# Optimization experiments

Hardware: AMD Instinct MI355X
Metric: run time of the kernel (lower is better)

## Reference

```python
import jax, jax.numpy as jnp
import numpy as np

B = 16384
S0, S1 = 7, 7
NB, NC = 2, 20
WC, WN = 5.0, 0.5  # weight_coord, weight_noobject
D = NB * 5 + NC  # 30


def setup_inputs() -> dict:
    key = jax.random.key(0)
    k1, k2, k3, k4 = jax.random.split(key, 4)
    predication = jax.random.normal(k1, (B, S0 * S1 * D), dtype=jnp.float32)
    grid = jax.random.randint(k2, (B, S0, S1), 0, 2, dtype=jnp.int32)
    tbox = jax.random.uniform(k3, (B, S0, S1, 4), dtype=jnp.float32)
    # keep target w,h strictly positive (real boxes), offsets in [0,1)
    tbox = tbox.at[..., 2:].set(0.05 + 0.9 * tbox[..., 2:])
    tcls = jax.random.randint(k4, (B, S0, S1), 0, NC, dtype=jnp.int32)
    return {"predication": predication, "grid": grid, "tbox": tbox, "tcls": tcls}


def _yolo_loss(predication, grid, tbox, tcls):
    pred = predication.reshape(B, S0, S1, D)
    conf = jax.nn.sigmoid(pred[..., :NB])                                  # (B,S0,S1,NB)
    pb = jax.nn.sigmoid(pred[..., NB:5 * NB]).reshape(B, S0, S1, NB, 4)    # (B,S0,S1,NB,4)
    cls = jax.nn.softmax(pred[..., 5 * NB:], axis=-1)                      # (B,S0,S1,NC)

    # cell coordinates: x = column index, y = row index (matches the [1,0] swap in torch code)
    xg = jnp.arange(S1, dtype=pred.dtype)[None, None, :]   # (1,1,S1)
    yg = jnp.arange(S0, dtype=pred.dtype)[None, :, None]   # (1,S0,1)

    tox, toy, tw, th = tbox[..., 0], tbox[..., 1], tbox[..., 2], tbox[..., 3]
    tcx = (xg + tox) / S0
    tcy = (yg + toy) / S1

    pcx = (xg[..., None] + pb[..., 0]) / S0   # (B,S0,S1,NB)
    pcy = (yg[..., None] + pb[..., 1]) / S1
    pw, ph = pb[..., 2], pb[..., 3]

    # IOU of each predicted box vs the cell's target box (same formula as _calc_iou)
    tb_ = jnp.minimum(tcx[..., None] + tw[..., None] / 2, pcx + pw / 2) - \
          jnp.maximum(tcx[..., None] - tw[..., None] / 2, pcx - pw / 2)
    lr_ = jnp.minimum(tcy[..., None] + th[..., None] / 2, pcy + ph / 2) - \
          jnp.maximum(tcy[..., None] - th[..., None] / 2, pcy - ph / 2)
    inter = jnp.where((tb_ < 0) | (lr_ < 0), 0.0, tb_ * lr_)
    iou = inter / ((tw * th)[..., None] + pw * ph - inter)                 # (B,S0,S1,NB)

    # best predictor chosen on detached IOUs (original uses pred_boxes.detach())
    best = jnp.argmax(jax.lax.stop_gradient(iou), axis=-1)                 # (B,S0,S1)

    take = lambda a: jnp.take_along_axis(a, best[..., None], axis=-1)[..., 0]
    iou_b = take(iou)          # attached IOU re-used in confidence loss
    conf_b = take(conf)
    pbb = jnp.take_along_axis(pb, best[..., None, None], axis=3)[..., 0, :]  # (B,S0,S1,4)

    cls_t = jnp.take_along_axis(cls, tcls[..., None], axis=-1)[..., 0]

    coord = (pbb[..., 0] - tox) ** 2 + (pbb[..., 1] - toy) ** 2 \
          + (jnp.sqrt(pbb[..., 2]) - jnp.sqrt(tw)) ** 2 \
          + (jnp.sqrt(pbb[..., 3]) - jnp.sqrt(th)) ** 2

    obj_loss = WC * coord + (conf_b - iou_b) ** 2 + (1.0 - cls_t) ** 2     # (B,S0,S1)
    noobj_loss = WN * jnp.sum(conf ** 2, axis=-1)                          # (B,S0,S1)

    objm = (grid == 1).astype(pred.dtype)
    total = jnp.sum(objm * obj_loss + (1.0 - objm) * noobj_loss)
    return total / B


def reference(predication, grid, tbox, tcls):
    return _yolo_loss(predication, grid, tbox, tcls)
```

## Files before the change

kernel.cpp:

```cpp
#include <hip/hip_runtime.h>
#include <math.h>

namespace {

constexpr int kB    = 16384;
constexpr int kS0   = 7;
constexpr int kS1   = 7;
constexpr int kD    = 30;
constexpr int kCells = kB * kS0 * kS1;
constexpr int TPB   = 256;
constexpr int NBLK  = kCells / TPB;
constexpr float kInv7 = 1.0f / 7.0f;
constexpr float kWC = 5.0f;
constexpr float kWN = 0.5f;

__device__ __forceinline__ float sigm(float x) {
    return 1.0f / (1.0f + __expf(-x));
}

__global__ void zero_out(float* out) {
    if (threadIdx.x == 0) out[0] = 0.0f;
}

__global__ void __launch_bounds__(TPB) yolo_loss_kernel(
    const float* __restrict__ pred,
    const int*   __restrict__ grid,
    const float* __restrict__ tbox,
    const int*   __restrict__ tcls,
    float* __restrict__ out)
{
    __shared__ float sp[TPB * kD];
    __shared__ float wsum[TPB / 64];

    const int tid  = threadIdx.x;
    const int cell0 = blockIdx.x * TPB;

    {
        const float4* __restrict__ g4 =
            reinterpret_cast<const float4*>(pred + (size_t)cell0 * kD);
        float4* s4 = reinterpret_cast<float4*>(sp);
        for (int i = tid; i < TPB * kD / 4; i += TPB) s4[i] = g4[i];
    }
    __syncthreads();

    const int cell = cell0 + tid;
    const int cj = cell % kS1;
    const int ci = (cell / kS1) % kS0;

    float f[kD];
    {
        const float2* p2 = reinterpret_cast<const float2*>(sp + tid * kD);
        #pragma unroll
        for (int q = 0; q < kD / 2; ++q) {
            float2 t = p2[q];
            f[2 * q]     = t.x;
            f[2 * q + 1] = t.y;
        }
    }

    const float4 tb4 = reinterpret_cast<const float4*>(tbox)[cell];
    const float tox = tb4.x, toy = tb4.y, tw = tb4.z, th = tb4.w;
    const int g  = grid[cell];
    const int tc = tcls[cell];

    const float conf0 = sigm(f[0]);
    const float conf1 = sigm(f[1]);
    float pbx[2], pby[2], pbw[2], pbh[2];
    #pragma unroll
    for (int k = 0; k < 2; ++k) {
        pbx[k] = sigm(f[2 + 4 * k + 0]);
        pby[k] = sigm(f[2 + 4 * k + 1]);
        pbw[k] = sigm(f[2 + 4 * k + 2]);
        pbh[k] = sigm(f[2 + 4 * k + 3]);
    }

    float cmax = f[10];
    #pragma unroll
    for (int q = 11; q < 30; ++q) cmax = fmaxf(cmax, f[q]);
    float csum = 0.0f, et = 0.0f;
    #pragma unroll
    for (int q = 0; q < 20; ++q) {
        const float e = __expf(f[10 + q] - cmax);
        csum += e;
        et = (q == tc) ? e : et;
    }
    const float cls_t = et / csum;

    const float x = (float)cj, y = (float)ci;
    const float tcx = (x + tox) * kInv7;
    const float tcy = (y + toy) * kInv7;
    const float thw = tw * 0.5f, thh = th * 0.5f;
    const float tarea = tw * th;

    float iou0, iou1;
    {
        const float pcx = (x + pbx[0]) * kInv7;
        const float pcy = (y + pby[0]) * kInv7;
        const float pw = pbw[0], ph = pbh[0];
        const float tb_ = fminf(tcx + thw, pcx + pw * 0.5f) - fmaxf(tcx - thw, pcx - pw * 0.5f);
        const float lr_ = fminf(tcy + thh, pcy + ph * 0.5f) - fmaxf(tcy - thh, pcy - ph * 0.5f);
        float inter = tb_ * lr_;
        inter = (tb_ < 0.0f || lr_ < 0.0f) ? 0.0f : inter;
        iou0 = inter / (tarea + pw * ph - inter);
    }
    {
        const float pcx = (x + pbx[1]) * kInv7;
        const float pcy = (y + pby[1]) * kInv7;
        const float pw = pbw[1], ph = pbh[1];
        const float tb_ = fminf(tcx + thw, pcx + pw * 0.5f) - fmaxf(tcx - thw, pcx - pw * 0.5f);
        const float lr_ = fminf(tcy + thh, pcy + ph * 0.5f) - fmaxf(tcy - thh, pcy - ph * 0.5f);
        float inter = tb_ * lr_;
        inter = (tb_ < 0.0f || lr_ < 0.0f) ? 0.0f : inter;
        iou1 = inter / (tarea + pw * ph - inter);
    }

    const bool b1 = (iou1 > iou0);
    const float bx = b1 ? pbx[1] : pbx[0];
    const float by = b1 ? pby[1] : pby[0];
    const float bw = b1 ? pbw[1] : pbw[0];
    const float bh = b1 ? pbh[1] : pbh[0];
    const float conf_b = b1 ? conf1 : conf0;
    const float iou_b  = b1 ? iou1  : iou0;

    const float dx = bx - tox;
    const float dy = by - toy;
    const float dw = sqrtf(bw) - sqrtf(tw);
    const float dh = sqrtf(bh) - sqrtf(th);
    const float coord = dx * dx + dy * dy + dw * dw + dh * dh;
    const float d1 = conf_b - iou_b;
    const float d2 = 1.0f - cls_t;
    const float obj   = kWC * coord + d1 * d1 + d2 * d2;
    const float noobj = kWN * (conf0 * conf0 + conf1 * conf1);

    float v = (g == 1) ? obj : noobj;

    #pragma unroll
    for (int off = 32; off > 0; off >>= 1) v += __shfl_down(v, off, 64);
    const int wave = tid >> 6;
    if ((tid & 63) == 0) wsum[wave] = v;
    __syncthreads();
    if (tid == 0) {
        const float s = wsum[0] + wsum[1] + wsum[2] + wsum[3];
        atomicAdd(out, s * (1.0f / kB));
    }
}

}

extern "C" void kernel_launch(void* const* d_in, const int* in_sizes, int n_in,
                              void* d_out, int out_size, void* d_ws, size_t ws_size,
                              hipStream_t stream) {
    const float* pred = (const float*)d_in[0];
    const int*   grid = (const int*)d_in[1];
    const float* tbox = (const float*)d_in[2];
    const int*   tcls = (const int*)d_in[3];
    float* out = (float*)d_out;

    zero_out<<<1, 64, 0, stream>>>(out);
    yolo_loss_kernel<<<NBLK, TPB, 0, stream>>>(pred, grid, tbox, tcls, out);
}
```

Baseline: 176.1 us.

## Process two cell tiles per block with all global loads issued up front

```diff
diff --git a/kernel.cpp b/kernel.cpp
--- a/kernel.cpp
+++ b/kernel.cpp
@@ -9,7 +9,8 @@
 constexpr int kD    = 30;
 constexpr int kCells = kB * kS0 * kS1;
 constexpr int TPB   = 256;
-constexpr int NBLK  = kCells / TPB;
+constexpr int CPB   = 512;
+constexpr int NBLK  = kCells / CPB;
 constexpr float kInv7 = 1.0f / 7.0f;
 constexpr float kWC = 5.0f;
 constexpr float kWN = 0.5f;
@@ -18,35 +19,9 @@
     return 1.0f / (1.0f + __expf(-x));
 }
 
-__global__ void zero_out(float* out) {
-    if (threadIdx.x == 0) out[0] = 0.0f;
-}
-
-__global__ void __launch_bounds__(TPB) yolo_loss_kernel(
-    const float* __restrict__ pred,
-    const int*   __restrict__ grid,
-    const float* __restrict__ tbox,
-    const int*   __restrict__ tcls,
-    float* __restrict__ out)
+__device__ __forceinline__ float cell_loss(const float* __restrict__ sp, int tid,
+                                           int cell, float4 tb4, int g, int tc)
 {
-    __shared__ float sp[TPB * kD];
-    __shared__ float wsum[TPB / 64];
-
-    const int tid  = threadIdx.x;
-    const int cell0 = blockIdx.x * TPB;
-
-    {
-        const float4* __restrict__ g4 =
-            reinterpret_cast<const float4*>(pred + (size_t)cell0 * kD);
-        float4* s4 = reinterpret_cast<float4*>(sp);
-        for (int i = tid; i < TPB * kD / 4; i += TPB) s4[i] = g4[i];
-    }
-    __syncthreads();
-
-    const int cell = cell0 + tid;
-    const int cj = cell % kS1;
-    const int ci = (cell / kS1) % kS0;
-
     float f[kD];
     {
         const float2* p2 = reinterpret_cast<const float2*>(sp + tid * kD);
@@ -58,10 +33,9 @@
         }
     }
 
-    const float4 tb4 = reinterpret_cast<const float4*>(tbox)[cell];
+    const int cj = cell % kS1;
+    const int ci = (cell / kS1) % kS0;
     const float tox = tb4.x, toy = tb4.y, tw = tb4.z, th = tb4.w;
-    const int g  = grid[cell];
-    const int tc = tcls[cell];
 
     const float conf0 = sigm(f[0]);
     const float conf1 = sigm(f[1]);
@@ -92,35 +66,26 @@
     const float thw = tw * 0.5f, thh = th * 0.5f;
     const float tarea = tw * th;
 
-    float iou0, iou1;
-    {
-        const float pcx = (x + pbx[0]) * kInv7;
-        const float pcy = (y + pby[0]) * kInv7;
-        const float pw = pbw[0], ph = pbh[0];
+    float iou[2];
+    #pragma unroll
+    for (int k = 0; k < 2; ++k) {
+        const float pcx = (x + pbx[k]) * kInv7;
+        const float pcy = (y + pby[k]) * kInv7;
+        const float pw = pbw[k], ph = pbh[k];
         const float tb_ = fminf(tcx + thw, pcx + pw * 0.5f) - fmaxf(tcx - thw, pcx - pw * 0.5f);
         const float lr_ = fminf(tcy + thh, pcy + ph * 0.5f) - fmaxf(tcy - thh, pcy - ph * 0.5f);
         float inter = tb_ * lr_;
         inter = (tb_ < 0.0f || lr_ < 0.0f) ? 0.0f : inter;
-        iou0 = inter / (tarea + pw * ph - inter);
-    }
-    {
-        const float pcx = (x + pbx[1]) * kInv7;
-        const float pcy = (y + pby[1]) * kInv7;
-        const float pw = pbw[1], ph = pbh[1];
-        const float tb_ = fminf(tcx + thw, pcx + pw * 0.5f) - fmaxf(tcx - thw, pcx - pw * 0.5f);
-        const float lr_ = fminf(tcy + thh, pcy + ph * 0.5f) - fmaxf(tcy - thh, pcy - ph * 0.5f);
-        float inter = tb_ * lr_;
-        inter = (tb_ < 0.0f || lr_ < 0.0f) ? 0.0f : inter;
-        iou1 = inter / (tarea + pw * ph - inter);
+        iou[k] = inter / (tarea + pw * ph - inter);
     }
 
-    const bool b1 = (iou1 > iou0);
+    const bool b1 = (iou[1] > iou[0]);
     const float bx = b1 ? pbx[1] : pbx[0];
     const float by = b1 ? pby[1] : pby[0];
     const float bw = b1 ? pbw[1] : pbw[0];
     const float bh = b1 ? pbh[1] : pbh[0];
     const float conf_b = b1 ? conf1 : conf0;
-    const float iou_b  = b1 ? iou1  : iou0;
+    const float iou_b  = b1 ? iou[1] : iou[0];
 
     const float dx = bx - tox;
     const float dy = by - toy;
@@ -132,16 +97,63 @@
     const float obj   = kWC * coord + d1 * d1 + d2 * d2;
     const float noobj = kWN * (conf0 * conf0 + conf1 * conf1);
 
-    float v = (g == 1) ? obj : noobj;
+    return (g == 1) ? obj : noobj;
+}
+
+__global__ void __launch_bounds__(TPB) yolo_loss_kernel(
+    const float* __restrict__ pred,
+    const int*   __restrict__ grid,
+    const float* __restrict__ tbox,
+    const int*   __restrict__ tcls,
+    float* __restrict__ out)
+{
+    __shared__ float sp[TPB * kD];
+    __shared__ float wsum[TPB / 64];
+
+    const int tid  = threadIdx.x;
+    const int base = blockIdx.x * CPB;
+    const int wave = tid >> 6;
+    const int lane = tid & 63;
+
+    const float4* __restrict__ g4 =
+        reinterpret_cast<const float4*>(pred + (size_t)base * kD);
+    float4* s4 = reinterpret_cast<float4*>(sp);
+    const bool extra = (tid < 128);
+
+    float4 r0[7], r1[7], r0e, r1e;
+    #pragma unroll
+    for (int k = 0; k < 7; ++k) r0[k] = g4[tid + 256 * k];
+    if (extra) r0e = g4[1792 + tid];
+    #pragma unroll
+    for (int k = 0; k < 7; ++k) r1[k] = g4[1920 + tid + 256 * k];
+    if (extra) r1e = g4[1920 + 1792 + tid];
+
+    const int cellA = base + tid;
+    const int cellB = base + TPB + tid;
+    const float4 tbA = reinterpret_cast<const float4*>(tbox)[cellA];
+    const float4 tbB = reinterpret_cast<const float4*>(tbox)[cellB];
+    const int gA = grid[cellA], gB = grid[cellB];
+    const int tcA = tcls[cellA], tcB = tcls[cellB];
+
+    #pragma unroll
+    for (int k = 0; k < 7; ++k) s4[tid + 256 * k] = r0[k];
+    if (extra) s4[1792 + tid] = r0e;
+    __syncthreads();
+    float v = cell_loss(sp, tid, cellA, tbA, gA, tcA);
+    __syncthreads();
+
+    #pragma unroll
+    for (int k = 0; k < 7; ++k) s4[tid + 256 * k] = r1[k];
+    if (extra) s4[1792 + tid] = r1e;
+    __syncthreads();
+    v += cell_loss(sp, tid, cellB, tbB, gB, tcB);
 
     #pragma unroll
     for (int off = 32; off > 0; off >>= 1) v += __shfl_down(v, off, 64);
-    const int wave = tid >> 6;
-    if ((tid & 63) == 0) wsum[wave] = v;
+    if (lane == 0) wsum[wave] = v;
     __syncthreads();
     if (tid == 0) {
-        const float s = wsum[0] + wsum[1] + wsum[2] + wsum[3];
-        atomicAdd(out, s * (1.0f / kB));
+        atomicAdd(out, (wsum[0] + wsum[1] + wsum[2] + wsum[3]) * (1.0f / kB));
     }
 }
 
@@ -156,6 +168,6 @@
     const int*   tcls = (const int*)d_in[3];
     float* out = (float*)d_out;
 
-    zero_out<<<1, 64, 0, stream>>>(out);
+    hipMemsetAsync(out, 0, sizeof(float), stream);
     yolo_loss_kernel<<<NBLK, TPB, 0, stream>>>(pred, grid, tbox, tcls, out);
 }
```

New measurement: 176.9 us. About the same (+0.5%).
